# Kernel tuning notes

Hardware: AMD Instinct MI355X
Metric: run time of the kernel (lower is better)

Reference implementation:

```python
import jax, jax.numpy as jnp
import numpy as np

N = 100000      # nodes
E = 3200000     # edges (avg degree 32)
F_IN = 16       # node_feature_size
R1, R2, R3 = 8, 16, 8   # gcn hidden sizes
N1 = 32                  # mlp hidden


def _lin(k, fan_in, shape):
    s = 1.0 / np.sqrt(fan_in)
    return jax.random.uniform(k, shape, minval=-s, maxval=s, dtype=jnp.float32)


def setup_inputs() -> dict:
    key = jax.random.key(0)
    ks = jax.random.split(key, 16)
    x = jax.random.normal(ks[0], (N, F_IN), dtype=jnp.float32)
    edge_index = jax.random.randint(ks[1], (2, E), 0, N, dtype=jnp.int64)
    return {
        "x": x,
        "edge_index": edge_index,
        # GraphConv k: out = mean_agg(x_j) @ W_rel + b + x @ W_root  (PyG GraphConv, lin_root bias=False)
        "W_rel1": _lin(ks[2], F_IN, (F_IN, R1)), "b1": _lin(ks[3], F_IN, (R1,)), "W_root1": _lin(ks[4], F_IN, (F_IN, R1)),
        "W_rel2": _lin(ks[5], R1, (R1, R2)),   "b2": _lin(ks[6], R1, (R2,)),   "W_root2": _lin(ks[7], R1, (R1, R2)),
        "W_rel3": _lin(ks[8], R2, (R2, R3)),   "b3": _lin(ks[9], R2, (R3,)),   "W_root3": _lin(ks[10], R2, (R2, R3)),
        "fc1_W": _lin(ks[11], R3, (R3, N1)), "fc1_b": _lin(ks[12], R3, (N1,)),
        "fc2_W": _lin(ks[13], N1, (N1, 1)),  "fc2_b": _lin(ks[14], N1, (1,)),
    }


def _graph_conv(x, src, dst, W_rel, b, W_root):
    # message: gather source features; aggregate: mean over incoming edges at dst
    n = x.shape[0]
    msg_sum = jax.ops.segment_sum(x[src], dst, num_segments=n)          # [N, F]
    cnt = jax.ops.segment_sum(jnp.ones(src.shape, x.dtype), dst, num_segments=n)
    mean = msg_sum / jnp.maximum(cnt, 1.0)[:, None]
    return mean @ W_rel + b + x @ W_root


def reference(x, edge_index, W_rel1, b1, W_root1, W_rel2, b2, W_root2,
              W_rel3, b3, W_root3, fc1_W, fc1_b, fc2_W, fc2_b):
    src, dst = edge_index[0], edge_index[1]
    h = jax.nn.sigmoid(_graph_conv(x, src, dst, W_rel1, b1, W_root1))
    h = jax.nn.sigmoid(_graph_conv(h, src, dst, W_rel2, b2, W_root2))
    h = jax.nn.sigmoid(_graph_conv(h, src, dst, W_rel3, b3, W_root3))
    h = jax.nn.sigmoid(h @ fc1_W + fc1_b)
    return h @ fc2_W + fc2_b   # [N, 1]
```

## Files before the change

kernel.cpp:

```cpp
#include <hip/hip_runtime.h>
#include <math.h>


#define CHUNK     8192
#define BW        128
#define MAXNB     800
#define MAXB_RAW  5376
#define MAXB_PAD  5760
#define REGION    5760

typedef _Float16 half8 __attribute__((ext_vector_type(8)));

static __device__ __forceinline__ float sigmoidf_(float x) {
    return 1.0f / (1.0f + expf(-x));
}

static __device__ __forceinline__ int scan256_excl(int v, int* s) {
    int tid = threadIdx.x;
    s[tid] = v;
    for (int off = 1; off < 256; off <<= 1) {
        __syncthreads();
        int t = (tid >= off) ? s[tid - off] : 0;
        __syncthreads();
        s[tid] += t;
    }
    __syncthreads();
    return s[tid] - v;
}

static __device__ __forceinline__ void gather_sum8(
    const half8* __restrict__ t, const int* __restrict__ csr,
    int rs, int from, int to, float* s) {
#pragma unroll
    for (int c = 0; c < 8; ++c) s[c] = 0.0f;
    int e = from;
    for (; e + 4 <= to; e += 4) {
        int4 ci = *(const int4*)(csr + rs + e);
        half8 v0 = t[ci.x]; half8 v1 = t[ci.y];
        half8 v2 = t[ci.z]; half8 v3 = t[ci.w];
#pragma unroll
        for (int c = 0; c < 8; ++c)
            s[c] += ((float)v0[c] + (float)v1[c]) + ((float)v2[c] + (float)v3[c]);
    }
    for (; e < to; ++e) {
        half8 v = t[csr[rs + e]];
#pragma unroll
        for (int c = 0; c < 8; ++c) s[c] += (float)v[c];
    }
}

static __device__ __forceinline__ void quad_gather_mean8(
    const half8* __restrict__ t, const int* __restrict__ csr,
    int rs, int d, int q, float* s) {
    int qs = ((d + 15) >> 4) << 2;
    int from = q * qs; if (from > d) from = d;
    int to = from + qs; if (to > d) to = d;
    gather_sum8(t, csr, rs, from, to, s);
#pragma unroll
    for (int c = 0; c < 8; ++c) s[c] += __shfl_xor(s[c], 1);
#pragma unroll
    for (int c = 0; c < 8; ++c) s[c] += __shfl_xor(s[c], 2);
    float inv = 1.0f / (float)(d > 0 ? d : 1);
#pragma unroll
    for (int c = 0; c < 8; ++c) s[c] *= inv;
}

__global__ __launch_bounds__(512)
void setup_scatter_kernel(const float* __restrict__ x, const float* __restrict__ Wrel,
                          const float* __restrict__ bias, const float* __restrict__ Wroot,
                          _Float16* __restrict__ t1, _Float16* __restrict__ z1,
                          const int* __restrict__ src, const int* __restrict__ dst,
                          int* __restrict__ gcur, unsigned* __restrict__ stage,
                          int N, int E, int NB, int nbT) {
    __shared__ float sWr[128], sWo[128], sb[8];
    __shared__ int s_hist[MAXNB];
    __shared__ int s_cur[MAXNB];
    int tid = threadIdx.x, blk = blockIdx.x;

    if (blk < nbT) {
        if (tid < 128) { sWr[tid] = Wrel[tid]; sWo[tid] = Wroot[tid]; }
        if (tid >= 128 && tid < 136) sb[tid - 128] = bias[tid - 128];
        __syncthreads();
        int node = blk * 512 + tid;
        if (node >= N) return;
        const float4* x4 = (const float4*)x;
        float xv[16];
#pragma unroll
        for (int k = 0; k < 4; ++k) {
            float4 v = x4[node * 4 + k];
            xv[4 * k] = v.x; xv[4 * k + 1] = v.y; xv[4 * k + 2] = v.z; xv[4 * k + 3] = v.w;
        }
        float ta[8], za[8];
#pragma unroll
        for (int j = 0; j < 8; ++j) { ta[j] = 0.0f; za[j] = sb[j]; }
#pragma unroll
        for (int f = 0; f < 16; ++f) {
            float xf = xv[f];
#pragma unroll
            for (int j = 0; j < 8; ++j) {
                ta[j] += xf * sWr[f * 8 + j];
                za[j] += xf * sWo[f * 8 + j];
            }
        }
        half8 th, zh;
#pragma unroll
        for (int j = 0; j < 8; ++j) { th[j] = (_Float16)ta[j]; zh[j] = (_Float16)za[j]; }
        ((half8*)t1)[node] = th;
        ((half8*)z1)[node] = zh;
    } else {
        int chunk = blk - nbT;
        int base = chunk * CHUNK;
        int cnt = E - base; if (cnt > CHUNK) cnt = CHUNK;
        for (int i = tid; i < NB; i += 512) s_hist[i] = 0;
        __syncthreads();
        if (cnt == CHUNK) {
            const int4* d4 = (const int4*)(dst + base);
#pragma unroll
            for (int k = 0; k < CHUNK / 2048; ++k) {
                int4 d = d4[k * 512 + tid];
                atomicAdd(&s_hist[d.x >> 7], 1);
                atomicAdd(&s_hist[d.y >> 7], 1);
                atomicAdd(&s_hist[d.z >> 7], 1);
                atomicAdd(&s_hist[d.w >> 7], 1);
            }
        } else {
            for (int i = tid; i < cnt; i += 512) atomicAdd(&s_hist[dst[base + i] >> 7], 1);
        }
        __syncthreads();
        for (int i = tid; i < NB; i += 512) {
            int hh = s_hist[i];
            s_cur[i] = i * REGION + atomicAdd(&gcur[i], hh);
        }
        __syncthreads();
        if (cnt == CHUNK) {
            const int4* d4 = (const int4*)(dst + base);
            const int4* s4 = (const int4*)(src + base);
#pragma unroll
            for (int k = 0; k < CHUNK / 2048; ++k) {
                int4 d = d4[k * 512 + tid];
                int4 s = s4[k * 512 + tid];
                int dd[4] = {d.x, d.y, d.z, d.w};
                int ss[4] = {s.x, s.y, s.z, s.w};
#pragma unroll
                for (int j = 0; j < 4; ++j) {
                    int pos = atomicAdd(&s_cur[dd[j] >> 7], 1);
                    stage[pos] = ((unsigned)(dd[j] & 127) << 17) | (unsigned)ss[j];
                }
            }
        } else {
            for (int i = tid; i < cnt; i += 512) {
                int d = dst[base + i], s = src[base + i];
                int pos = atomicAdd(&s_cur[d >> 7], 1);
                stage[pos] = ((unsigned)(d & 127) << 17) | (unsigned)s;
            }
        }
    }
}

__global__ __launch_bounds__(256)
void csr_agg1_kernel(const unsigned* __restrict__ stage, const int* __restrict__ gcur,
                     int* __restrict__ csr, int* __restrict__ deg,
                     int* __restrict__ rowstart,
                     const _Float16* __restrict__ t1, const _Float16* __restrict__ z1,
                     _Float16* __restrict__ h1, int N) {
    __shared__ unsigned __attribute__((aligned(16))) s_p[MAXB_RAW];
    __shared__ int __attribute__((aligned(16))) s_out[MAXB_PAD];
    __shared__ int h[BW], hs[BW], curb[BW];
    __shared__ int s_scan[256];
    int b = blockIdx.x, tid = threadIdx.x;
    int beg = b * REGION;
    int tot = gcur[b]; if (tot > MAXB_RAW) tot = MAXB_RAW;

    const uint4* st4 = (const uint4*)(stage + beg);
    int n4 = tot >> 2;
    for (int i = tid; i < n4; i += 256) ((uint4*)s_p)[i] = st4[i];
    for (int i = (n4 << 2) + tid; i < tot; i += 256) s_p[i] = stage[beg + i];
    if (tid < BW) h[tid] = 0;
    __syncthreads();

    for (int i = tid; i < tot; i += 256) atomicAdd(&h[s_p[i] >> 17], 1);
    __syncthreads();

    int v = (tid < BW) ? ((h[tid] + 3) & ~3) : 0;
    int excl = scan256_excl(v, s_scan);
    int ptot = s_scan[255];
    int dg = 0, myStart = 0;
    if (tid < BW) {
        dg = h[tid]; myStart = excl;
        hs[tid] = myStart; curb[tid] = myStart;
        int node = b * BW + tid;
        if (node < N) { deg[node] = dg; rowstart[node] = beg + myStart; }
    }
    __syncthreads();

    for (int i = tid; i < tot; i += 256) {
        unsigned p = s_p[i];
        int pos = atomicAdd(&curb[p >> 17], 1);
        s_out[pos] = (int)(p & 0x1FFFF);
    }
    __syncthreads();

    if (ptot > MAXB_PAD) ptot = MAXB_PAD;
    int p4 = ptot >> 2;
    int4* csr4 = (int4*)(csr + beg);
    for (int i = tid; i < p4; i += 256) csr4[i] = ((const int4*)s_out)[i];

    int nd = tid >> 1, half = tid & 1;
    int node = b * BW + nd;
    if (node < N) {
        int rs = hs[nd], d = h[nd];
        int d1 = ((d >> 1) + 3) & ~3; if (d1 > d) d1 = d;
        int from = half ? d1 : 0;
        int to   = half ? d  : d1;
        const half8* t = (const half8*)t1;
        float s[8];
#pragma unroll
        for (int c = 0; c < 8; ++c) s[c] = 0.0f;
        int e = from;
        for (; e + 4 <= to; e += 4) {
            int4 ci = *(const int4*)(s_out + rs + e);
            half8 v0 = t[ci.x]; half8 v1 = t[ci.y];
            half8 v2 = t[ci.z]; half8 v3 = t[ci.w];
#pragma unroll
            for (int c = 0; c < 8; ++c)
                s[c] += ((float)v0[c] + (float)v1[c]) + ((float)v2[c] + (float)v3[c]);
        }
        for (; e < to; ++e) {
            half8 vv = t[s_out[rs + e]];
#pragma unroll
            for (int c = 0; c < 8; ++c) s[c] += (float)vv[c];
        }
#pragma unroll
        for (int c = 0; c < 8; ++c) s[c] += __shfl_xor(s[c], 1);
        if (half == 0) {
            float inv = 1.0f / (float)(d > 0 ? d : 1);
            half8 z = ((const half8*)z1)[node];
            half8 o;
#pragma unroll
            for (int c = 0; c < 8; ++c) o[c] = (_Float16)sigmoidf_(s[c] * inv + (float)z[c]);
            ((half8*)h1)[node] = o;
        }
    }
}

__global__ __launch_bounds__(256)
void gcn2_fused_kernel(const _Float16* __restrict__ h1,
                       const int* __restrict__ rowstart, const int* __restrict__ deg,
                       const int* __restrict__ csr,
                       const float* __restrict__ W2r, const float* __restrict__ b2,
                       const float* __restrict__ W2o,
                       const float* __restrict__ W3r, const float* __restrict__ b3,
                       const float* __restrict__ W3o,
                       _Float16* __restrict__ t3, _Float16* __restrict__ z3, int n) {
    __shared__ float sW2r[128], sW2o[128], sW3r[128], sW3o[128], sb2[16], sb3[8];
    int tid = threadIdx.x;
    if (tid < 128) {
        sW2r[tid] = W2r[tid]; sW2o[tid] = W2o[tid];
        sW3r[tid] = W3r[tid]; sW3o[tid] = W3o[tid];
    }
    if (tid < 16) sb2[tid] = b2[tid];
    if (tid < 8) sb3[tid] = b3[tid];
    __syncthreads();
    int idx = blockIdx.x * 256 + tid;
    int node = idx >> 2, q = idx & 3;
    if (node >= n) return;

    float m[8];
    quad_gather_mean8((const half8*)h1, csr, rowstart[node], deg[node], q, m);
    half8 sf = ((const half8*)h1)[node];
    float x8[8];
#pragma unroll
    for (int c = 0; c < 8; ++c) x8[c] = (float)sf[c];

    float v16[16];
#pragma unroll
    for (int j = 0; j < 16; ++j) {
        float a = sb2[j];
#pragma unroll
        for (int f = 0; f < 8; ++f)
            a += m[f] * sW2r[f * 16 + j] + x8[f] * sW2o[f * 16 + j];
        v16[j] = sigmoidf_(a);
    }
    float ta[8], za[8];
#pragma unroll
    for (int j = 0; j < 8; ++j) { ta[j] = 0.0f; za[j] = sb3[j]; }
#pragma unroll
    for (int f = 0; f < 16; ++f) {
        float hv = v16[f];
#pragma unroll
        for (int j = 0; j < 8; ++j) {
            ta[j] += hv * sW3r[f * 8 + j];
            za[j] += hv * sW3o[f * 8 + j];
        }
    }
    if (q) return;
    half8 th, zh;
#pragma unroll
    for (int j = 0; j < 8; ++j) { th[j] = (_Float16)ta[j]; zh[j] = (_Float16)za[j]; }
    ((half8*)t3)[node] = th;
    ((half8*)z3)[node] = zh;
}

__global__ __launch_bounds__(256)
void agg3_mlp_kernel(const _Float16* __restrict__ t3, const _Float16* __restrict__ z3,
                     const int* __restrict__ rowstart, const int* __restrict__ deg,
                     const int* __restrict__ csr,
                     const float* __restrict__ fc1W, const float* __restrict__ fc1b,
                     const float* __restrict__ fc2W, const float* __restrict__ fc2b,
                     float* __restrict__ out, int n) {
    __shared__ float sW1[256], sb1[32], sW2[32];
    __shared__ float sb2_;
    int tid = threadIdx.x;
    if (tid < 256) sW1[tid] = fc1W[tid];
    if (tid < 32) { sb1[tid] = fc1b[tid]; sW2[tid] = fc2W[tid]; }
    if (tid == 0) sb2_ = fc2b[0];
    __syncthreads();
    int idx = blockIdx.x * 256 + tid;
    int node = idx >> 2, q = idx & 3;
    if (node >= n) return;

    float s[8];
    quad_gather_mean8((const half8*)t3, csr, rowstart[node], deg[node], q, s);
    half8 z = ((const half8*)z3)[node];
    float h[8];
#pragma unroll
    for (int c = 0; c < 8; ++c) h[c] = sigmoidf_(s[c] + (float)z[c]);

    float acc = sb2_;
#pragma unroll
    for (int j = 0; j < 32; ++j) {
        float a = sb1[j];
#pragma unroll
        for (int f = 0; f < 8; ++f) a += h[f] * sW1[f * 32 + j];
        acc += sW2[j] * sigmoidf_(a);
    }
    if (q == 0) out[node] = acc;
}

extern "C" void kernel_launch(void* const* d_in, const int* in_sizes, int n_in,
                              void* d_out, int out_size, void* d_ws, size_t ws_size,
                              hipStream_t stream) {
    const float* x      = (const float*)d_in[0];
    const int*   ei     = (const int*)d_in[1];
    const float* Wrel1  = (const float*)d_in[2];
    const float* b1     = (const float*)d_in[3];
    const float* Wroot1 = (const float*)d_in[4];
    const float* Wrel2  = (const float*)d_in[5];
    const float* b2     = (const float*)d_in[6];
    const float* Wroot2 = (const float*)d_in[7];
    const float* Wrel3  = (const float*)d_in[8];
    const float* b3     = (const float*)d_in[9];
    const float* Wroot3 = (const float*)d_in[10];
    const float* fc1W   = (const float*)d_in[11];
    const float* fc1b   = (const float*)d_in[12];
    const float* fc2W   = (const float*)d_in[13];
    const float* fc2b   = (const float*)d_in[14];
    float* out = (float*)d_out;

    const int N = in_sizes[0] / 16;
    const int E = in_sizes[1] / 2;
    const int* e_src = ei;
    const int* e_dst = ei + E;

    const int NB   = (N + BW - 1) / BW;
    const int NBLK = (E + CHUNK - 1) / CHUNK;
    const int nbT  = (N + 511) / 512;
    const int nbQ  = (4 * N + 255) / 256;

    char* ws = (char*)d_ws;
    size_t off = 0;
    auto alloc = [&](size_t bytes) { char* p = ws + off; off += (bytes + 15) & ~size_t(15); return p; };
    unsigned* stage = (unsigned*)alloc((size_t)NB * REGION * 4);
    int* csr        = (int*)alloc((size_t)NB * REGION * 4);
    int* gcur       = (int*)alloc((size_t)NB * 4);
    int* deg        = (int*)alloc((size_t)N * 4);
    int* rowstart   = (int*)alloc((size_t)N * 4);
    _Float16* t1    = (_Float16*)alloc((size_t)N * 8 * 2);
    _Float16* z1    = (_Float16*)alloc((size_t)N * 8 * 2);
    _Float16* h1    = (_Float16*)alloc((size_t)N * 8 * 2);
    _Float16* t3    = (_Float16*)alloc((size_t)N * 8 * 2);
    _Float16* z3    = (_Float16*)alloc((size_t)N * 8 * 2);

    hipMemsetAsync(gcur, 0, (size_t)NB * 4, stream);

    setup_scatter_kernel<<<nbT + NBLK, 512, 0, stream>>>(
        x, Wrel1, b1, Wroot1, t1, z1, e_src, e_dst, gcur, stage, N, E, NB, nbT);
    csr_agg1_kernel<<<NB, 256, 0, stream>>>(stage, gcur, csr, deg, rowstart,
                                            t1, z1, h1, N);
    gcn2_fused_kernel<<<nbQ, 256, 0, stream>>>(h1, rowstart, deg, csr,
                                               Wrel2, b2, Wroot2, Wrel3, b3, Wroot3, t3, z3, N);
    agg3_mlp_kernel<<<nbQ, 256, 0, stream>>>(t3, z3, rowstart, deg, csr,
                                             fc1W, fc1b, fc2W, fc2b, out, N);
}
```

Before: 226.7 us.

## Switch layer-2/3 aggregation to edge-parallel slot segments with shared-memory atomics

Replaces the node-parallel quad gather in the layer-2 and layer-3 kernels with edge-parallel processing per 128-node bucket. Each thread takes 12 consecutive CSR slots, issues all gathers up front, finds its starting node by binary search, and flushes running sums into shared-memory accumulators with atomics. The aim is to even out load imbalance from varying degrees and to raise memory-level parallelism. In exchange it adds shared atomics, a zero-fill of the padded CSR slots, a per-bucket slot count array, and only 128 of 512 threads doing the dense MLP tail.

```diff
diff --git a/kernel.cpp b/kernel.cpp
--- a/kernel.cpp
+++ b/kernel.cpp
@@ -8,6 +8,7 @@
 #define MAXB_RAW  5376
 #define MAXB_PAD  5760
 #define REGION    5760
+#define SLT       12
 
 typedef _Float16 half8 __attribute__((ext_vector_type(8)));
 
@@ -26,43 +27,6 @@
     }
     __syncthreads();
     return s[tid] - v;
-}
-
-static __device__ __forceinline__ void gather_sum8(
-    const half8* __restrict__ t, const int* __restrict__ csr,
-    int rs, int from, int to, float* s) {
-#pragma unroll
-    for (int c = 0; c < 8; ++c) s[c] = 0.0f;
-    int e = from;
-    for (; e + 4 <= to; e += 4) {
-        int4 ci = *(const int4*)(csr + rs + e);
-        half8 v0 = t[ci.x]; half8 v1 = t[ci.y];
-        half8 v2 = t[ci.z]; half8 v3 = t[ci.w];
-#pragma unroll
-        for (int c = 0; c < 8; ++c)
-            s[c] += ((float)v0[c] + (float)v1[c]) + ((float)v2[c] + (float)v3[c]);
-    }
-    for (; e < to; ++e) {
-        half8 v = t[csr[rs + e]];
-#pragma unroll
-        for (int c = 0; c < 8; ++c) s[c] += (float)v[c];
-    }
-}
-
-static __device__ __forceinline__ void quad_gather_mean8(
-    const half8* __restrict__ t, const int* __restrict__ csr,
-    int rs, int d, int q, float* s) {
-    int qs = ((d + 15) >> 4) << 2;
-    int from = q * qs; if (from > d) from = d;
-    int to = from + qs; if (to > d) to = d;
-    gather_sum8(t, csr, rs, from, to, s);
-#pragma unroll
-    for (int c = 0; c < 8; ++c) s[c] += __shfl_xor(s[c], 1);
-#pragma unroll
-    for (int c = 0; c < 8; ++c) s[c] += __shfl_xor(s[c], 2);
-    float inv = 1.0f / (float)(d > 0 ? d : 1);
-#pragma unroll
-    for (int c = 0; c < 8; ++c) s[c] *= inv;
 }
 
 __global__ __launch_bounds__(512)
@@ -160,7 +124,7 @@
 __global__ __launch_bounds__(256)
 void csr_agg1_kernel(const unsigned* __restrict__ stage, const int* __restrict__ gcur,
                      int* __restrict__ csr, int* __restrict__ deg,
-                     int* __restrict__ rowstart,
+                     int* __restrict__ rowstart, int* __restrict__ ptot_arr,
                      const _Float16* __restrict__ t1, const _Float16* __restrict__ z1,
                      _Float16* __restrict__ h1, int N) {
     __shared__ unsigned __attribute__((aligned(16))) s_p[MAXB_RAW];
@@ -183,7 +147,7 @@
 
     int v = (tid < BW) ? ((h[tid] + 3) & ~3) : 0;
     int excl = scan256_excl(v, s_scan);
-    int ptot = s_scan[255];
+    int ptot = s_scan[255]; if (ptot > MAXB_PAD) ptot = MAXB_PAD;
     int dg = 0, myStart = 0;
     if (tid < BW) {
         dg = h[tid]; myStart = excl;
@@ -191,6 +155,8 @@
         int node = b * BW + tid;
         if (node < N) { deg[node] = dg; rowstart[node] = beg + myStart; }
     }
+    if (tid == 0) ptot_arr[b] = ptot;
+    for (int i = tid; i < ptot; i += 256) s_out[i] = 0;
     __syncthreads();
 
     for (int i = tid; i < tot; i += 256) {
@@ -200,7 +166,6 @@
     }
     __syncthreads();
 
-    if (ptot > MAXB_PAD) ptot = MAXB_PAD;
     int p4 = ptot >> 2;
     int4* csr4 = (int4*)(csr + beg);
     for (int i = tid; i < p4; i += 256) csr4[i] = ((const int4*)s_out)[i];
@@ -243,98 +208,181 @@
     }
 }
 
-__global__ __launch_bounds__(256)
-void gcn2_fused_kernel(const _Float16* __restrict__ h1,
-                       const int* __restrict__ rowstart, const int* __restrict__ deg,
-                       const int* __restrict__ csr,
-                       const float* __restrict__ W2r, const float* __restrict__ b2,
-                       const float* __restrict__ W2o,
-                       const float* __restrict__ W3r, const float* __restrict__ b3,
-                       const float* __restrict__ W3o,
-                       _Float16* __restrict__ t3, _Float16* __restrict__ z3, int n) {
+static __device__ __forceinline__ void edge_accum(
+    const half8* __restrict__ t, const int* __restrict__ csr, int beg, int ptot,
+    const int* rsl, const int* dgl, float* acc) {
+    int tid = threadIdx.x;
+    int s0 = tid * SLT;
+    if (s0 >= ptot) return;
+    int sE = s0 + SLT; if (sE > ptot) sE = ptot;
+
+    half8 g[SLT];
+#pragma unroll
+    for (int j = 0; j < SLT; ++j) {
+        if (s0 + j < sE) g[j] = t[csr[beg + s0 + j]];
+    }
+
+    int lo = 0, hi = 127;
+    while (lo < hi) { int mid = (lo + hi + 1) >> 1; if (rsl[mid] <= s0) lo = mid; else hi = mid - 1; }
+    int nd = lo;
+
+    float run[8];
+#pragma unroll
+    for (int c = 0; c < 8; ++c) run[c] = 0.0f;
+    bool dirty = false;
+#pragma unroll
+    for (int j = 0; j < SLT; ++j) {
+        int slot = s0 + j;
+        if (slot >= sE) break;
+        while (slot >= rsl[nd + 1]) {
+            if (dirty) {
+#pragma unroll
+                for (int c = 0; c < 8; ++c) { atomicAdd(&acc[nd * 9 + c], run[c]); run[c] = 0.0f; }
+                dirty = false;
+            }
+            ++nd;
+        }
+        if (slot - rsl[nd] < dgl[nd]) {
+#pragma unroll
+            for (int c = 0; c < 8; ++c) run[c] += (float)g[j][c];
+            dirty = true;
+        }
+    }
+    if (dirty) {
+#pragma unroll
+        for (int c = 0; c < 8; ++c) atomicAdd(&acc[nd * 9 + c], run[c]);
+    }
+}
+
+__global__ __launch_bounds__(512)
+void gcn2_edge_kernel(const _Float16* __restrict__ h1,
+                      const int* __restrict__ rowstart, const int* __restrict__ deg,
+                      const int* __restrict__ csr, const int* __restrict__ ptot_arr,
+                      const float* __restrict__ W2r, const float* __restrict__ b2,
+                      const float* __restrict__ W2o,
+                      const float* __restrict__ W3r, const float* __restrict__ b3,
+                      const float* __restrict__ W3o,
+                      _Float16* __restrict__ t3, _Float16* __restrict__ z3, int N) {
     __shared__ float sW2r[128], sW2o[128], sW3r[128], sW3o[128], sb2[16], sb3[8];
-    int tid = threadIdx.x;
-    if (tid < 128) {
-        sW2r[tid] = W2r[tid]; sW2o[tid] = W2o[tid];
-        sW3r[tid] = W3r[tid]; sW3o[tid] = W3o[tid];
-    }
+    __shared__ float acc[BW * 9];
+    __shared__ int rsl[BW + 1], dgl[BW];
+    __shared__ int ptot_s;
+    int b = blockIdx.x, tid = threadIdx.x;
+    int beg = b * REGION;
+
+    if (tid == 0) ptot_s = ptot_arr[b];
+    if (tid < 128) { sW2r[tid] = W2r[tid]; sW2o[tid] = W2o[tid];
+                     sW3r[tid] = W3r[tid]; sW3o[tid] = W3o[tid]; }
     if (tid < 16) sb2[tid] = b2[tid];
-    if (tid < 8) sb3[tid] = b3[tid];
-    __syncthreads();
-    int idx = blockIdx.x * 256 + tid;
-    int node = idx >> 2, q = idx & 3;
-    if (node >= n) return;
-
-    float m[8];
-    quad_gather_mean8((const half8*)h1, csr, rowstart[node], deg[node], q, m);
-    half8 sf = ((const half8*)h1)[node];
-    float x8[8];
-#pragma unroll
-    for (int c = 0; c < 8; ++c) x8[c] = (float)sf[c];
-
-    float v16[16];
-#pragma unroll
-    for (int j = 0; j < 16; ++j) {
-        float a = sb2[j];
-#pragma unroll
-        for (int f = 0; f < 8; ++f)
-            a += m[f] * sW2r[f * 16 + j] + x8[f] * sW2o[f * 16 + j];
-        v16[j] = sigmoidf_(a);
-    }
-    float ta[8], za[8];
-#pragma unroll
-    for (int j = 0; j < 8; ++j) { ta[j] = 0.0f; za[j] = sb3[j]; }
-#pragma unroll
-    for (int f = 0; f < 16; ++f) {
-        float hv = v16[f];
-#pragma unroll
-        for (int j = 0; j < 8; ++j) {
-            ta[j] += hv * sW3r[f * 8 + j];
-            za[j] += hv * sW3o[f * 8 + j];
-        }
-    }
-    if (q) return;
-    half8 th, zh;
-#pragma unroll
-    for (int j = 0; j < 8; ++j) { th[j] = (_Float16)ta[j]; zh[j] = (_Float16)za[j]; }
-    ((half8*)t3)[node] = th;
-    ((half8*)z3)[node] = zh;
-}
-
-__global__ __launch_bounds__(256)
-void agg3_mlp_kernel(const _Float16* __restrict__ t3, const _Float16* __restrict__ z3,
-                     const int* __restrict__ rowstart, const int* __restrict__ deg,
-                     const int* __restrict__ csr,
-                     const float* __restrict__ fc1W, const float* __restrict__ fc1b,
-                     const float* __restrict__ fc2W, const float* __restrict__ fc2b,
-                     float* __restrict__ out, int n) {
+    if (tid < 8)  sb3[tid] = b3[tid];
+    for (int i = tid; i < BW * 9; i += 512) acc[i] = 0.0f;
+    __syncthreads();
+    int ptot = ptot_s;
+    if (tid < BW) {
+        int node = b * BW + tid;
+        rsl[tid] = (node < N) ? (rowstart[node] - beg) : ptot;
+        dgl[tid] = (node < N) ? deg[node] : 0;
+    }
+    if (tid == 0) rsl[BW] = ptot;
+    __syncthreads();
+
+    edge_accum((const half8*)h1, csr, beg, ptot, rsl, dgl, acc);
+    __syncthreads();
+
+    if (tid < BW) {
+        int node = b * BW + tid;
+        if (node < N) {
+            int d = dgl[tid];
+            float inv = 1.0f / (float)(d > 0 ? d : 1);
+            float m[8];
+#pragma unroll
+            for (int c = 0; c < 8; ++c) m[c] = acc[tid * 9 + c] * inv;
+            half8 sf = ((const half8*)h1)[node];
+            float x8[8];
+#pragma unroll
+            for (int c = 0; c < 8; ++c) x8[c] = (float)sf[c];
+            float v16[16];
+#pragma unroll
+            for (int j = 0; j < 16; ++j) {
+                float a = sb2[j];
+#pragma unroll
+                for (int f = 0; f < 8; ++f)
+                    a += m[f] * sW2r[f * 16 + j] + x8[f] * sW2o[f * 16 + j];
+                v16[j] = sigmoidf_(a);
+            }
+            float ta[8], za[8];
+#pragma unroll
+            for (int j = 0; j < 8; ++j) { ta[j] = 0.0f; za[j] = sb3[j]; }
+#pragma unroll
+            for (int f = 0; f < 16; ++f) {
+                float hv = v16[f];
+#pragma unroll
+                for (int j = 0; j < 8; ++j) {
+                    ta[j] += hv * sW3r[f * 8 + j];
+                    za[j] += hv * sW3o[f * 8 + j];
+                }
+            }
+            half8 th, zh;
+#pragma unroll
+            for (int j = 0; j < 8; ++j) { th[j] = (_Float16)ta[j]; zh[j] = (_Float16)za[j]; }
+            ((half8*)t3)[node] = th;
+            ((half8*)z3)[node] = zh;
+        }
+    }
+}
+
+__global__ __launch_bounds__(512)
+void agg3_edge_kernel(const _Float16* __restrict__ t3, const _Float16* __restrict__ z3,
+                      const int* __restrict__ rowstart, const int* __restrict__ deg,
+                      const int* __restrict__ csr, const int* __restrict__ ptot_arr,
+                      const float* __restrict__ fc1W, const float* __restrict__ fc1b,
+                      const float* __restrict__ fc2W, const float* __restrict__ fc2b,
+                      float* __restrict__ out, int N) {
     __shared__ float sW1[256], sb1[32], sW2[32];
     __shared__ float sb2_;
-    int tid = threadIdx.x;
+    __shared__ float acc[BW * 9];
+    __shared__ int rsl[BW + 1], dgl[BW];
+    __shared__ int ptot_s;
+    int b = blockIdx.x, tid = threadIdx.x;
+    int beg = b * REGION;
+
+    if (tid == 0) { ptot_s = ptot_arr[b]; sb2_ = fc2b[0]; }
     if (tid < 256) sW1[tid] = fc1W[tid];
     if (tid < 32) { sb1[tid] = fc1b[tid]; sW2[tid] = fc2W[tid]; }
-    if (tid == 0) sb2_ = fc2b[0];
-    __syncthreads();
-    int idx = blockIdx.x * 256 + tid;
-    int node = idx >> 2, q = idx & 3;
-    if (node >= n) return;
-
-    float s[8];
-    quad_gather_mean8((const half8*)t3, csr, rowstart[node], deg[node], q, s);
-    half8 z = ((const half8*)z3)[node];
-    float h[8];
-#pragma unroll
-    for (int c = 0; c < 8; ++c) h[c] = sigmoidf_(s[c] + (float)z[c]);
-
-    float acc = sb2_;
-#pragma unroll
-    for (int j = 0; j < 32; ++j) {
-        float a = sb1[j];
-#pragma unroll
-        for (int f = 0; f < 8; ++f) a += h[f] * sW1[f * 32 + j];
-        acc += sW2[j] * sigmoidf_(a);
-    }
-    if (q == 0) out[node] = acc;
+    for (int i = tid; i < BW * 9; i += 512) acc[i] = 0.0f;
+    __syncthreads();
+    int ptot = ptot_s;
+    if (tid < BW) {
+        int node = b * BW + tid;
+        rsl[tid] = (node < N) ? (rowstart[node] - beg) : ptot;
+        dgl[tid] = (node < N) ? deg[node] : 0;
+    }
+    if (tid == 0) rsl[BW] = ptot;
+    __syncthreads();
+
+    edge_accum((const half8*)t3, csr, beg, ptot, rsl, dgl, acc);
+    __syncthreads();
+
+    if (tid < BW) {
+        int node = b * BW + tid;
+        if (node < N) {
+            int d = dgl[tid];
+            float inv = 1.0f / (float)(d > 0 ? d : 1);
+            half8 z = ((const half8*)z3)[node];
+            float h[8];
+#pragma unroll
+            for (int c = 0; c < 8; ++c) h[c] = sigmoidf_(acc[tid * 9 + c] * inv + (float)z[c]);
+            float a2 = sb2_;
+#pragma unroll
+            for (int j = 0; j < 32; ++j) {
+                float a = sb1[j];
+#pragma unroll
+                for (int f = 0; f < 8; ++f) a += h[f] * sW1[f * 32 + j];
+                a2 += sW2[j] * sigmoidf_(a);
+            }
+            out[node] = a2;
+        }
+    }
 }
 
 extern "C" void kernel_launch(void* const* d_in, const int* in_sizes, int n_in,
@@ -365,7 +413,6 @@
     const int NB   = (N + BW - 1) / BW;
     const int NBLK = (E + CHUNK - 1) / CHUNK;
     const int nbT  = (N + 511) / 512;
-    const int nbQ  = (4 * N + 255) / 256;
 
     char* ws = (char*)d_ws;
     size_t off = 0;
@@ -375,6 +422,7 @@
     int* gcur       = (int*)alloc((size_t)NB * 4);
     int* deg        = (int*)alloc((size_t)N * 4);
     int* rowstart   = (int*)alloc((size_t)N * 4);
+    int* ptot_arr   = (int*)alloc((size_t)NB * 4);
     _Float16* t1    = (_Float16*)alloc((size_t)N * 8 * 2);
     _Float16* z1    = (_Float16*)alloc((size_t)N * 8 * 2);
     _Float16* h1    = (_Float16*)alloc((size_t)N * 8 * 2);
@@ -386,9 +434,10 @@
     setup_scatter_kernel<<<nbT + NBLK, 512, 0, stream>>>(
         x, Wrel1, b1, Wroot1, t1, z1, e_src, e_dst, gcur, stage, N, E, NB, nbT);
     csr_agg1_kernel<<<NB, 256, 0, stream>>>(stage, gcur, csr, deg, rowstart,
-                                            t1, z1, h1, N);
-    gcn2_fused_kernel<<<nbQ, 256, 0, stream>>>(h1, rowstart, deg, csr,
-                                               Wrel2, b2, Wroot2, Wrel3, b3, Wroot3, t3, z3, N);
-    agg3_mlp_kernel<<<nbQ, 256, 0, stream>>>(t3, z3, rowstart, deg, csr,
+                                            ptot_arr, t1, z1, h1, N);
+    gcn2_edge_kernel<<<NB, 512, 0, stream>>>(h1, rowstart, deg, csr, ptot_arr,
+                                             Wrel2, b2, Wroot2, Wrel3, b3, Wroot3,
+                                             t3, z3, N);
+    agg3_edge_kernel<<<NB, 512, 0, stream>>>(t3, z3, rowstart, deg, csr, ptot_arr,
                                              fc1W, fc1b, fc2W, fc2b, out, N);
 }
```

Measured after the change: 282.7 us. 24.7% more time.
